# Kernel tuning notes

Measured on AMD Instinct MI355X. Metric: run time of the kernel, lower is better.

## Reference

```python
import jax, jax.numpy as jnp
import numpy as np

IN_FEATURES = 8192
OUT_FEATURES = 8192
MAX_STATES = 100
THRESHOLD = MAX_STATES // 2  # 50


def setup_inputs() -> dict:
    key = jax.random.key(0)
    k1, k2, k3, k4 = jax.random.split(key, 4)
    # mimic module init: states = randn*2 + threshold, clamped to [1, max_states]
    synapse_states = jnp.clip(
        jax.random.normal(k1, (OUT_FEATURES, IN_FEATURES), dtype=jnp.float32) * 2.0 + THRESHOLD,
        1.0, float(MAX_STATES))
    spike_input = (jax.random.uniform(k2, (IN_FEATURES,), dtype=jnp.float32) > 0.5).astype(jnp.float32)
    # non-trivial running state so all update paths are exercised
    membrane_potential = jax.random.uniform(k3, (OUT_FEATURES,), dtype=jnp.float32) * 4.0
    adaptive_threshold = jnp.full((OUT_FEATURES,), 5.0, dtype=jnp.float32)
    eligibility_trace = jax.random.uniform(k4, (OUT_FEATURES, IN_FEATURES), dtype=jnp.float32)
    return {
        "spike_input": spike_input,
        "synapse_states": synapse_states,
        "membrane_potential": membrane_potential,
        "adaptive_threshold": adaptive_threshold,
        "eligibility_trace": eligibility_trace,
    }


def reference(spike_input, synapse_states, membrane_potential, adaptive_threshold, eligibility_trace):
    # ternary (here effectively binary 0/1) weights from integer-like synapse states
    w = (synapse_states > THRESHOLD).astype(jnp.float32)  # [O, I]
    x = spike_input.reshape(-1)                           # [I]
    current = w @ x                                       # [O] (x @ w.T flattened)
    # membrane decay + integrate
    v_mem = membrane_potential * 0.9 + current            # [O]
    spikes = (v_mem >= adaptive_threshold).astype(jnp.float32)
    # eligibility trace: decay + outer-product Hebbian term, clamped
    new_trace = jnp.clip(eligibility_trace * 0.8 + jnp.outer(spikes, x), 0.0, 5.0)
    # homeostatic threshold adaptation
    new_threshold = jnp.clip(adaptive_threshold + (spikes - 0.1) * 0.1, 1.0, 20.0)
    # reset membrane where spiked, leaky retain otherwise
    new_membrane = v_mem * (1.0 - spikes) * 0.1
    return spikes, new_membrane, new_threshold, new_trace
```

## Files before the change

### kernel.cpp

```cpp
#include <hip/hip_runtime.h>


constexpr int O_FEAT = 8192;
constexpr int I_FEAT = 8192;
constexpr float STATE_THR = 50.0f;

typedef float f32x4 __attribute__((ext_vector_type(4)));

__global__ __launch_bounds__(256) void snn_fused_v5(
    const float* __restrict__ x,
    const float* __restrict__ syn,
    const float* __restrict__ mp,
    const float* __restrict__ thr,
    const float* __restrict__ tr,
    float* __restrict__ out)
{
    const int t = threadIdx.x;
    const int o = blockIdx.x;
    const long long rowoff = (long long)o * I_FEAT;

    const f32x4* __restrict__ x4 = (const f32x4*)x;
    const f32x4* __restrict__ s4 = (const f32x4*)(syn + rowoff);
    const f32x4* __restrict__ t4 = (const f32x4*)(tr + rowoff);
    f32x4* __restrict__ n4 = (f32x4*)(out + 3LL * O_FEAT + rowoff);

    const float mpv = mp[o];
    const float th  = thr[o];

    unsigned xmask = 0u, smask = 0u;
#pragma unroll
    for (int j = 0; j < 8; ++j) {
        const int idx = j * 256 + t;
        const f32x4 xv = x4[idx];
        const f32x4 sv = s4[idx];
        const unsigned xn = (xv.x != 0.0f ? 1u : 0u) | (xv.y != 0.0f ? 2u : 0u)
                          | (xv.z != 0.0f ? 4u : 0u) | (xv.w != 0.0f ? 8u : 0u);
        const unsigned sn = (sv.x > STATE_THR ? 1u : 0u) | (sv.y > STATE_THR ? 2u : 0u)
                          | (sv.z > STATE_THR ? 4u : 0u) | (sv.w > STATE_THR ? 8u : 0u);
        xmask |= xn << (j * 4);
        smask |= sn << (j * 4);
    }
    int cnt = __popc(xmask & smask);

    const f32x4 tp0 = t4[t];
    const f32x4 tp1 = t4[256 + t];

#pragma unroll
    for (int off = 1; off < 64; off <<= 1)
        cnt += __shfl_xor(cnt, off, 64);

    __shared__ int wsum[4];
    if ((t & 63) == 0) wsum[t >> 6] = cnt;
    __syncthreads();
    const int total = ((wsum[0] + wsum[1]) + wsum[2]) + wsum[3];

    const float v_mem = __fadd_rn(__fmul_rn(mpv, 0.9f), (float)total);
    const float s = (v_mem >= th) ? 1.0f : 0.0f;
    if (t == 0) {
        out[o] = s;
        out[O_FEAT + o] = __fmul_rn(__fmul_rn(v_mem, 1.0f - s), 0.1f);
        float nth = __fadd_rn(th, __fmul_rn(s - 0.1f, 0.1f));
        out[2 * O_FEAT + o] = fminf(fmaxf(nth, 1.0f), 20.0f);
    }

#pragma unroll
    for (int j = 0; j < 8; ++j) {
        const int idx = j * 256 + t;
        const f32x4 tv = (j == 0) ? tp0 : (j == 1) ? tp1 : t4[idx];
        const unsigned mb = xmask >> (j * 4);
        f32x4 r;
        r.x = fminf(fmaxf(__fadd_rn(__fmul_rn(tv.x, 0.8f), (mb & 1u) ? s : 0.0f), 0.0f), 5.0f);
        r.y = fminf(fmaxf(__fadd_rn(__fmul_rn(tv.y, 0.8f), (mb & 2u) ? s : 0.0f), 0.0f), 5.0f);
        r.z = fminf(fmaxf(__fadd_rn(__fmul_rn(tv.z, 0.8f), (mb & 4u) ? s : 0.0f), 0.0f), 5.0f);
        r.w = fminf(fmaxf(__fadd_rn(__fmul_rn(tv.w, 0.8f), (mb & 8u) ? s : 0.0f), 0.0f), 5.0f);
        __builtin_nontemporal_store(r, &n4[idx]);
    }
}

extern "C" void kernel_launch(void* const* d_in, const int* in_sizes, int n_in,
                              void* d_out, int out_size, void* d_ws, size_t ws_size,
                              hipStream_t stream) {
    const float* x   = (const float*)d_in[0];
    const float* syn = (const float*)d_in[1];
    const float* mp  = (const float*)d_in[2];
    const float* th  = (const float*)d_in[3];
    const float* tr  = (const float*)d_in[4];
    float* out = (float*)d_out;

    snn_fused_v5<<<O_FEAT, 256, 0, stream>>>(x, syn, mp, th, tr, out);
}
```

Measured before the change: 139.1 us.

## Split fused kernel into spike-computation and trace-update kernels

Splits the single fused kernel into two launches. The first computes spikes with one wavefront per output row, which removes the block-level shared-memory reduction and barrier. The second reads the spike from global output and streams the eligibility trace update. This decouples the trace stream from the reduction barrier, at the cost of an extra launch, re-reading x per element instead of using a bitmask, and losing any overlap between the synapse and trace reads within one block.

Result: no change. 141.6 us (+1.8%).

```diff
diff --git a/kernel.cpp b/kernel.cpp
--- a/kernel.cpp
+++ b/kernel.cpp
@@ -7,11 +7,52 @@
 
 typedef float f32x4 __attribute__((ext_vector_type(4)));
 
-__global__ __launch_bounds__(256) void snn_fused_v5(
+__global__ __launch_bounds__(256) void snn_p1_spikes(
     const float* __restrict__ x,
     const float* __restrict__ syn,
     const float* __restrict__ mp,
     const float* __restrict__ thr,
+    float* __restrict__ out)
+{
+    const int lane = threadIdx.x & 63;
+    const int o = (blockIdx.x * blockDim.x + threadIdx.x) >> 6;
+    const long long rowoff = (long long)o * I_FEAT;
+
+    const f32x4* __restrict__ x4 = (const f32x4*)x;
+    const f32x4* __restrict__ s4 = (const f32x4*)(syn + rowoff);
+
+    const float mpv = mp[o];
+    const float th  = thr[o];
+
+    int cnt = 0;
+#pragma unroll 8
+    for (int j = 0; j < 32; ++j) {
+        const int idx = j * 64 + lane;
+        const f32x4 sv = s4[idx];
+        const f32x4 xv = x4[idx];
+        const unsigned sn = (sv.x > STATE_THR ? 1u : 0u) | (sv.y > STATE_THR ? 2u : 0u)
+                          | (sv.z > STATE_THR ? 4u : 0u) | (sv.w > STATE_THR ? 8u : 0u);
+        const unsigned xn = (xv.x != 0.0f ? 1u : 0u) | (xv.y != 0.0f ? 2u : 0u)
+                          | (xv.z != 0.0f ? 4u : 0u) | (xv.w != 0.0f ? 8u : 0u);
+        cnt += __popc(sn & xn);
+    }
+
+#pragma unroll
+    for (int off = 1; off < 64; off <<= 1)
+        cnt += __shfl_xor(cnt, off, 64);
+
+    const float v_mem = __fadd_rn(__fmul_rn(mpv, 0.9f), (float)cnt);
+    const float s = (v_mem >= th) ? 1.0f : 0.0f;
+    if (lane == 0) {
+        out[o] = s;
+        out[O_FEAT + o] = __fmul_rn(__fmul_rn(v_mem, 1.0f - s), 0.1f);
+        float nth = __fadd_rn(th, __fmul_rn(s - 0.1f, 0.1f));
+        out[2 * O_FEAT + o] = fminf(fmaxf(nth, 1.0f), 20.0f);
+    }
+}
+
+__global__ __launch_bounds__(256) void snn_p2_trace(
+    const float* __restrict__ x,
     const float* __restrict__ tr,
     float* __restrict__ out)
 {
@@ -20,59 +61,21 @@
     const long long rowoff = (long long)o * I_FEAT;
 
     const f32x4* __restrict__ x4 = (const f32x4*)x;
-    const f32x4* __restrict__ s4 = (const f32x4*)(syn + rowoff);
     const f32x4* __restrict__ t4 = (const f32x4*)(tr + rowoff);
     f32x4* __restrict__ n4 = (f32x4*)(out + 3LL * O_FEAT + rowoff);
 
-    const float mpv = mp[o];
-    const float th  = thr[o];
-
-    unsigned xmask = 0u, smask = 0u;
-#pragma unroll
-    for (int j = 0; j < 8; ++j) {
-        const int idx = j * 256 + t;
-        const f32x4 xv = x4[idx];
-        const f32x4 sv = s4[idx];
-        const unsigned xn = (xv.x != 0.0f ? 1u : 0u) | (xv.y != 0.0f ? 2u : 0u)
-                          | (xv.z != 0.0f ? 4u : 0u) | (xv.w != 0.0f ? 8u : 0u);
-        const unsigned sn = (sv.x > STATE_THR ? 1u : 0u) | (sv.y > STATE_THR ? 2u : 0u)
-                          | (sv.z > STATE_THR ? 4u : 0u) | (sv.w > STATE_THR ? 8u : 0u);
-        xmask |= xn << (j * 4);
-        smask |= sn << (j * 4);
-    }
-    int cnt = __popc(xmask & smask);
-
-    const f32x4 tp0 = t4[t];
-    const f32x4 tp1 = t4[256 + t];
-
-#pragma unroll
-    for (int off = 1; off < 64; off <<= 1)
-        cnt += __shfl_xor(cnt, off, 64);
-
-    __shared__ int wsum[4];
-    if ((t & 63) == 0) wsum[t >> 6] = cnt;
-    __syncthreads();
-    const int total = ((wsum[0] + wsum[1]) + wsum[2]) + wsum[3];
-
-    const float v_mem = __fadd_rn(__fmul_rn(mpv, 0.9f), (float)total);
-    const float s = (v_mem >= th) ? 1.0f : 0.0f;
-    if (t == 0) {
-        out[o] = s;
-        out[O_FEAT + o] = __fmul_rn(__fmul_rn(v_mem, 1.0f - s), 0.1f);
-        float nth = __fadd_rn(th, __fmul_rn(s - 0.1f, 0.1f));
-        out[2 * O_FEAT + o] = fminf(fmaxf(nth, 1.0f), 20.0f);
-    }
+    const float s = out[o];
 
 #pragma unroll
     for (int j = 0; j < 8; ++j) {
         const int idx = j * 256 + t;
-        const f32x4 tv = (j == 0) ? tp0 : (j == 1) ? tp1 : t4[idx];
-        const unsigned mb = xmask >> (j * 4);
+        const f32x4 tv = t4[idx];
+        const f32x4 xv = x4[idx];
         f32x4 r;
-        r.x = fminf(fmaxf(__fadd_rn(__fmul_rn(tv.x, 0.8f), (mb & 1u) ? s : 0.0f), 0.0f), 5.0f);
-        r.y = fminf(fmaxf(__fadd_rn(__fmul_rn(tv.y, 0.8f), (mb & 2u) ? s : 0.0f), 0.0f), 5.0f);
-        r.z = fminf(fmaxf(__fadd_rn(__fmul_rn(tv.z, 0.8f), (mb & 4u) ? s : 0.0f), 0.0f), 5.0f);
-        r.w = fminf(fmaxf(__fadd_rn(__fmul_rn(tv.w, 0.8f), (mb & 8u) ? s : 0.0f), 0.0f), 5.0f);
+        r.x = fminf(fmaxf(__fadd_rn(__fmul_rn(tv.x, 0.8f), (xv.x != 0.0f) ? s : 0.0f), 0.0f), 5.0f);
+        r.y = fminf(fmaxf(__fadd_rn(__fmul_rn(tv.y, 0.8f), (xv.y != 0.0f) ? s : 0.0f), 0.0f), 5.0f);
+        r.z = fminf(fmaxf(__fadd_rn(__fmul_rn(tv.z, 0.8f), (xv.z != 0.0f) ? s : 0.0f), 0.0f), 5.0f);
+        r.w = fminf(fmaxf(__fadd_rn(__fmul_rn(tv.w, 0.8f), (xv.w != 0.0f) ? s : 0.0f), 0.0f), 5.0f);
         __builtin_nontemporal_store(r, &n4[idx]);
     }
 }
@@ -87,5 +90,6 @@
     const float* tr  = (const float*)d_in[4];
     float* out = (float*)d_out;
 
-    snn_fused_v5<<<O_FEAT, 256, 0, stream>>>(x, syn, mp, th, tr, out);
+    snn_p1_spikes<<<O_FEAT / 4, 256, 0, stream>>>(x, syn, mp, th, out);
+    snn_p2_trace<<<O_FEAT, 256, 0, stream>>>(x, tr, out);
 }
```
